# Optimization experiments

Measured on AMD Instinct MI355X. Metric: run time of the kernel, lower is better.

The kernel has to match this reference:

```python
import jax, jax.numpy as jnp
import numpy as np

N_HEAD, D_K, D_V, D_MODEL = 8, 64, 64, 512
LN_EPS = 1e-5

def setup_inputs() -> dict:
    key = jax.random.key(0)
    k1, k2, k3 = jax.random.split(key, 3)
    B, C, H, W = 8, D_MODEL, 32, 32
    q = jax.random.normal(k1, (B, C, H, W), dtype=jnp.float32)
    w_qkvs = jax.random.normal(k2, (N_HEAD * D_K, D_MODEL), dtype=jnp.float32) * np.sqrt(2.0 / (D_MODEL + D_K))
    fc_w = jax.random.normal(k3, (D_MODEL, N_HEAD * D_V), dtype=jnp.float32) * np.sqrt(2.0 / (N_HEAD * D_V + D_MODEL))
    fc_b = jnp.zeros((D_MODEL,), dtype=jnp.float32)
    ln_gamma = jnp.ones((D_MODEL,), dtype=jnp.float32)
    ln_beta = jnp.zeros((D_MODEL,), dtype=jnp.float32)
    return {"q": q, "w_qkvs": w_qkvs, "fc_w": fc_w, "fc_b": fc_b,
            "ln_gamma": ln_gamma, "ln_beta": ln_beta}

def reference(q, w_qkvs, fc_w, fc_b, ln_gamma, ln_beta):
    B, C, H, W = q.shape
    L = H * W
    temp = np.sqrt(D_K).astype(np.float32)
    # [B, C, H, W] -> [B, L, C] tokens
    x = q.reshape(B, C, L).transpose(0, 2, 1)
    residual = x
    # shared QKV projection -> per-head [B, h, L, d]
    qh = (x @ w_qkvs.T).reshape(B, L, N_HEAD, D_K).transpose(0, 2, 1, 3)
    # self-attention: q = k = v = qh
    scores = jnp.einsum('bhqd,bhkd->bhqk', qh, qh) / temp
    attn = jax.nn.softmax(scores, axis=-1)  # dropout is identity in eval
    out = jnp.einsum('bhqk,bhkd->bhqd', attn, qh)  # [B, h, L, d_v]
    # merge heads: [B, L, h*d_v]
    out = out.transpose(0, 2, 1, 3).reshape(B, L, N_HEAD * D_V)
    out = out @ fc_w.T + fc_b
    y = out + residual
    mu = jnp.mean(y, axis=-1, keepdims=True)
    var = jnp.mean(jnp.square(y - mu), axis=-1, keepdims=True)
    y = (y - mu) / jnp.sqrt(var + LN_EPS) * ln_gamma + ln_beta
    # raw reshape, matching torch .view(B, -1, H, W)
    return y.reshape(B, -1, H, W)
```

## Files before the change

kernel.cpp:

```cpp
#include <hip/hip_runtime.h>
#include <stdint.h>

#define BATCH 8
#define LTOK 1024
#define DMODEL 512
#define NHEAD 8
#define DHEAD 64

typedef unsigned short u16;
typedef u16 u16x4 __attribute__((ext_vector_type(4)));
typedef u16 u16x8 __attribute__((ext_vector_type(8)));
typedef short bf16x8 __attribute__((ext_vector_type(8)));
typedef float f32x4 __attribute__((ext_vector_type(4)));

#define MFMA16(a,b,c) __builtin_amdgcn_mfma_f32_16x16x32_bf16((a),(b),(c),0,0,0)

__device__ __forceinline__ float bf2f(u16 x){
  union{unsigned u; float f;} v; v.u = ((unsigned)x)<<16; return v.f;
}
__device__ __forceinline__ u16 f2bf(float f){
  union{float f; unsigned u;} v; v.f = f;
  unsigned r = v.u + 0x7fffu + ((v.u>>16)&1u);
  return (u16)(r>>16);
}

__device__ __forceinline__ void gload_lds16(const u16* g, u16* l){
  __builtin_amdgcn_global_load_lds(
      (const __attribute__((address_space(1))) void*)g,
      (__attribute__((address_space(3))) void*)l,
      16, 0, 0);
}

__global__ __launch_bounds__(256) void prep_k(const float* __restrict__ q,
                                              u16* __restrict__ x_rm,
                                              const float* __restrict__ w0,
                                              u16* __restrict__ d0,
                                              const float* __restrict__ w1,
                                              u16* __restrict__ d1){
  __shared__ __align__(16) u16 t[64][72];
  const int blk = blockIdx.x;
  const int tid = threadIdx.x;
  if (blk < 1024){
    const int bx = blk & 7, by = (blk>>3) & 15, bz = blk>>7;
    const int r0 = bx*64, c0 = by*64;
    const float* s = q    + (size_t)bz*DMODEL*LTOK;
    u16* d         = x_rm + (size_t)bz*DMODEL*LTOK;
    const int row = tid>>3, ch = (tid&7)*8;
    #pragma unroll
    for (int rr=0; rr<64; rr+=32){
      const float* p = s + (size_t)(r0+row+rr)*LTOK + c0 + ch;
      u16x8 v;
      #pragma unroll
      for (int j=0;j<8;j++) v[j] = f2bf(p[j]);
      *(u16x8*)&t[row+rr][ch] = v;
    }
    __syncthreads();
    #pragma unroll
    for (int rr=0; rr<64; rr+=32){
      const int dr = row+rr;
      u16x8 v;
      #pragma unroll
      for (int j=0;j<8;j++) v[j] = t[ch+j][dr];
      *(u16x8*)(d + (size_t)(c0+dr)*DMODEL + r0 + ch) = v;
    }
  } else {
    const int b2 = blk - 1024;
    const float* src = (b2 < 128) ? w0 : w1;
    u16* dst        = (b2 < 128) ? d0 : d1;
    const int i = (((b2 & 127)*256) + tid)*8;
    u16x8 v;
    #pragma unroll
    for (int j=0;j<8;j++) v[j] = f2bf(src[i+j]);
    *(u16x8*)(dst + i) = v;
  }
}

__device__ __forceinline__ void stage128(const u16* __restrict__ src,
                                         int row0, int k0, u16* lds, int tid){
  #pragma unroll
  for (int s2=0; s2<4; ++s2){
    const int slot = tid + s2*256;
    const int row = slot>>3, ch8 = slot&7;
    const int k = k0 + ((ch8 ^ (row&7))<<3);
    gload_lds16(src + (size_t)(row0+row)*DMODEL + k, lds + slot*8);
  }
}

__global__ __launch_bounds__(256) void qkv_gemm(const u16* __restrict__ A,
                                                const u16* __restrict__ W,
                                                u16* __restrict__ Kf,
                                                u16* __restrict__ Vf){
  __shared__ __align__(128) u16 smem[32768];
  const int m0 = blockIdx.x*128, n0 = blockIdx.y*128;
  const int tid = threadIdx.x, w = tid>>6, lane = tid&63;
  const int wr = w>>1, wc = w&1;
  const int lr = lane&15, lg = lane>>4;
  f32x4 acc[4][4] = {};
  stage128(A, m0, 0, smem, tid);
  stage128(W, n0, 0, smem + 16384, tid);
  int buf = 0;
  for (int kt=0; kt<8; ++kt){
    __syncthreads();
    if (kt < 7){
      stage128(A, m0, (kt+1)*64, smem + (buf^1)*8192, tid);
      stage128(W, n0, (kt+1)*64, smem + 16384 + (buf^1)*8192, tid);
    }
    const u16* sa = smem + buf*8192;
    const u16* sb = smem + 16384 + buf*8192;
    #pragma unroll
    for (int ks=0; ks<2; ++ks){
      bf16x8 af[4], bfr[4];
      #pragma unroll
      for (int mi=0; mi<4; ++mi){
        const int r = wr*64 + mi*16 + lr;
        af[mi] = *(const bf16x8*)(&sa[(r*64 + ks*32 + lg*8) ^ ((r&7)<<3)]);
      }
      #pragma unroll
      for (int nj=0; nj<4; ++nj){
        const int r = wc*64 + nj*16 + lr;
        bfr[nj] = *(const bf16x8*)(&sb[(r*64 + ks*32 + lg*8) ^ ((r&7)<<3)]);
      }
      #pragma unroll
      for (int mi=0; mi<4; ++mi)
        #pragma unroll
        for (int nj=0; nj<4; ++nj)
          acc[mi][nj] = MFMA16(af[mi], bfr[nj], acc[mi][nj]);
    }
    buf ^= 1;
  }
  __syncthreads();
  u16* Ktile = smem + w*4096;
  u16* Vtile = smem + 16384 + w*4096;
  #pragma unroll
  for (int mi=0; mi<4; ++mi)
    #pragma unroll
    for (int nj=0; nj<4; ++nj){
      const int rrb = mi*16 + lg*4;
      const int d   = nj*16 + lr;
      #pragma unroll
      for (int r=0; r<4; ++r){
        const int rr = rrb + r;
        Ktile[((d>>5)*4 + (rr>>4))*512 + (((d>>3)&3)*16 + (rr&15))*8 + (d&7)]
            = f2bf(acc[mi][nj][r]);
      }
      u16x4 pv;
      #pragma unroll
      for (int r=0; r<4; ++r) pv[r] = f2bf(acc[mi][nj][r]);
      *(u16x4*)&Vtile[((rrb>>5)*4 + (d>>4))*512 + (((rrb>>3)&3)*16 + (d&15))*8 + (rrb&7)] = pv;
    }
  __syncthreads();
  const int bb = m0>>10, t0 = (m0&1023)>>6, hh0 = n0>>6;
  #pragma unroll
  for (int p=0; p<8; ++p){
    const int gi = p*2048 + tid*8;
    const int lt = gi>>12, off = gi&4095;
    const size_t base = (size_t)((bb*NHEAD + hh0 + (lt&1))*16 + t0 + (lt>>1))*4096 + off;
    *(u16x8*)(Kf + base) = *(const u16x8*)(smem + gi);
    *(u16x8*)(Vf + base) = *(const u16x8*)(smem + 16384 + gi);
  }
}

__global__ __launch_bounds__(256,2) void attn_k(const u16* __restrict__ kf,
                                                const u16* __restrict__ vf,
                                                u16* __restrict__ ao){
  __shared__ __align__(16) u16 sPm[16640];
  const int bid = blockIdx.x;
  const int qt = bid >> 6, bh = bid & 63;
  const int b = bh >> 3, h = bh & 7;
  const u16* Kf = kf + (size_t)bh*16*4096;
  const u16* Vf = vf + (size_t)bh*16*4096;
  const int tid = threadIdx.x, w = tid>>6, lane = tid&63;
  const int lr = lane&15, lg = lane>>4;

  bf16x8 aq[4][2];
  #pragma unroll
  for (int g=0; g<4; ++g)
    #pragma unroll
    for (int ks=0; ks<2; ++ks){
      u16x8 v = *(const u16x8*)(Kf + (size_t)qt*4096 + (ks*4+g)*512 + lane*8);
      bf16x8 t;
      #pragma unroll
      for (int j=0;j<8;j++) t[j] = (short)f2bf(bf2f(v[j])*0.18033688f);
      aq[g][ks] = t;
    }

  f32x4 o[4][4] = {};
  float lsum[4][4] = {};

  for (int t=0; t<4; ++t){
    const int kt = w + t*4;
    const u16* Kt = Kf + (size_t)kt*4096;
    const u16* Vt = Vf + (size_t)kt*4096;
    bf16x8 bk[2][4];
    #pragma unroll
    for (int ks=0; ks<2; ++ks)
      #pragma unroll
      for (int nj=0; nj<4; ++nj)
        bk[ks][nj] = *(const bf16x8*)(Kt + (ks*4+nj)*512 + lane*8);
    #pragma unroll
    for (int g=0; g<4; ++g){
      f32x4 sc[4] = {};
      __builtin_amdgcn_s_setprio(1);
      #pragma unroll
      for (int ks=0; ks<2; ++ks)
        #pragma unroll
        for (int nj=0; nj<4; ++nj)
          sc[nj] = MFMA16(aq[g][ks], bk[ks][nj], sc[nj]);
      __builtin_amdgcn_s_setprio(0);
      const int wp = (w*4+g)*1024;
      #pragma unroll
      for (int nj=0; nj<4; ++nj){
        #pragma unroll
        for (int r=0; r<4; ++r){
          const float p = __builtin_amdgcn_exp2f(sc[nj][r]);
          lsum[g][r] += p;
          const int prow = lg*4 + r;
          sPm[wp + ((prow*64 + nj*16 + lr) ^ ((prow&7)<<3))]
              = (u16)(__float_as_uint(p)>>16);
        }
      }
    }
    asm volatile("s_waitcnt lgkmcnt(0)" ::: "memory");
    bf16x8 bv[2][4];
    #pragma unroll
    for (int ks=0; ks<2; ++ks)
      #pragma unroll
      for (int dj=0; dj<4; ++dj)
        bv[ks][dj] = *(const bf16x8*)(Vt + (ks*4+dj)*512 + lane*8);
    __builtin_amdgcn_s_setprio(1);
    #pragma unroll
    for (int g=0; g<4; ++g){
      const int wp = (w*4+g)*1024;
      #pragma unroll
      for (int ks=0; ks<2; ++ks){
        bf16x8 pa = *(const bf16x8*)(&sPm[wp + ((lr*64 + ks*32 + lg*8) ^ ((lr&7)<<3))]);
        #pragma unroll
        for (int dj=0; dj<4; ++dj)
          o[g][dj] = MFMA16(pa, bv[ks][dj], o[g][dj]);
      }
    }
    __builtin_amdgcn_s_setprio(0);
  }

  #pragma unroll
  for (int g=0; g<4; ++g)
    #pragma unroll
    for (int r=0; r<4; ++r){
      float s = lsum[g][r];
      s += __shfl_xor(s,1); s += __shfl_xor(s,2);
      s += __shfl_xor(s,4); s += __shfl_xor(s,8);
      lsum[g][r] = s;
    }

  __syncthreads();
  float* mrg = (float*)sPm;
  if (w & 1){
    float* R = mrg + (w>>1)*4160;
    #pragma unroll
    for (int g=0; g<4; ++g){
      #pragma unroll
      for (int dj=0; dj<4; ++dj)
        *(f32x4*)&R[(g*4+dj)*256 + lane*4] = o[g][dj];
      if (lr == 0)
        #pragma unroll
        for (int r=0; r<4; ++r) R[4096 + g*16 + lg*4 + r] = lsum[g][r];
    }
  }
  __syncthreads();
  if (!(w & 1)){
    float* R = mrg + (w>>1)*4160;
    #pragma unroll
    for (int g=0; g<4; ++g){
      #pragma unroll
      for (int dj=0; dj<4; ++dj)
        o[g][dj] += *(const f32x4*)&R[(g*4+dj)*256 + lane*4];
      #pragma unroll
      for (int r=0; r<4; ++r) lsum[g][r] += R[4096 + g*16 + lg*4 + r];
    }
  }
  if (w == 2){
    float* R = mrg + 4160;
    #pragma unroll
    for (int g=0; g<4; ++g){
      #pragma unroll
      for (int dj=0; dj<4; ++dj)
        *(f32x4*)&R[(g*4+dj)*256 + lane*4] = o[g][dj];
      if (lr == 0)
        #pragma unroll
        for (int r=0; r<4; ++r) R[4096 + g*16 + lg*4 + r] = lsum[g][r];
    }
  }
  __syncthreads();
  if (w == 0){
    float* R = mrg + 4160;
    #pragma unroll
    for (int g=0; g<4; ++g){
      #pragma unroll
      for (int dj=0; dj<4; ++dj)
        o[g][dj] += *(const f32x4*)&R[(g*4+dj)*256 + lane*4];
      #pragma unroll
      for (int r=0; r<4; ++r) lsum[g][r] += R[4096 + g*16 + lg*4 + r];
    }
    #pragma unroll
    for (int g=0; g<4; ++g){
      float inv[4];
      #pragma unroll
      for (int r=0; r<4; ++r) inv[r] = __builtin_amdgcn_rcpf(lsum[g][r]);
      const int i0 = qt*64 + g*16;
      #pragma unroll
      for (int dj=0; dj<4; ++dj)
        #pragma unroll
        for (int r=0; r<4; ++r){
          const int l = i0 + lg*4 + r;
          const int d = dj*16 + lr;
          ao[((size_t)(b*LTOK + l))*DMODEL + h*DHEAD + d] = f2bf(o[g][dj][r]*inv[r]);
        }
    }
  }
}

__global__ __launch_bounds__(256) void fc_gemm(const u16* __restrict__ A,
                                               const u16* __restrict__ W,
                                               const float* __restrict__ bias,
                                               const u16* __restrict__ resid,
                                               u16* __restrict__ Y){
  __shared__ __align__(128) u16 smem[32768];
  const int m0 = blockIdx.x*128, n0 = blockIdx.y*128;
  const int tid = threadIdx.x, w = tid>>6, lane = tid&63;
  const int wr = w>>1, wc = w&1;
  const int lr = lane&15, lg = lane>>4;
  f32x4 acc[4][4] = {};
  stage128(A, m0, 0, smem, tid);
  stage128(W, n0, 0, smem + 16384, tid);
  int buf = 0;
  for (int kt=0; kt<8; ++kt){
    __syncthreads();
    if (kt < 7){
      stage128(A, m0, (kt+1)*64, smem + (buf^1)*8192, tid);
      stage128(W, n0, (kt+1)*64, smem + 16384 + (buf^1)*8192, tid);
    }
    const u16* sa = smem + buf*8192;
    const u16* sb = smem + 16384 + buf*8192;
    #pragma unroll
    for (int ks=0; ks<2; ++ks){
      bf16x8 af[4], bfr[4];
      #pragma unroll
      for (int mi=0; mi<4; ++mi){
        const int r = wr*64 + mi*16 + lr;
        af[mi] = *(const bf16x8*)(&sa[(r*64 + ks*32 + lg*8) ^ ((r&7)<<3)]);
      }
      #pragma unroll
      for (int nj=0; nj<4; ++nj){
        const int r = wc*64 + nj*16 + lr;
        bfr[nj] = *(const bf16x8*)(&sb[(r*64 + ks*32 + lg*8) ^ ((r&7)<<3)]);
      }
      #pragma unroll
      for (int mi=0; mi<4; ++mi)
        #pragma unroll
        for (int nj=0; nj<4; ++nj)
          acc[mi][nj] = MFMA16(af[mi], bfr[nj], acc[mi][nj]);
    }
    buf ^= 1;
  }
  __syncthreads();
  float* lY = (float*)smem;
  #pragma unroll
  for (int mi=0; mi<4; ++mi)
    #pragma unroll
    for (int nj=0; nj<4; ++nj)
      #pragma unroll
      for (int r=0; r<4; ++r){
        const int rr = wr*64 + mi*16 + lg*4 + r;
        const int d  = wc*64 + nj*16 + lr;
        lY[rr*128 + (d ^ ((rr&7)<<2))] = acc[mi][nj][r];
      }
  __syncthreads();
  #pragma unroll
  for (int p=0; p<8; ++p){
    const int slot = p*256 + tid;
    const int row = slot>>4;
    const int ch  = (slot&15)*8;
    const int x   = (row&7)<<2;
    f32x4 ya = *(const f32x4*)&lY[row*128 + (ch ^ x)];
    f32x4 yb = *(const f32x4*)&lY[row*128 + ((ch+4) ^ x)];
    u16x8 rs = *(const u16x8*)(resid + (size_t)(m0+row)*DMODEL + n0 + ch);
    u16x8 o8;
    #pragma unroll
    for (int j=0;j<4;j++) o8[j]   = f2bf(ya[j] + bias[n0+ch+j]   + bf2f(rs[j]));
    #pragma unroll
    for (int j=0;j<4;j++) o8[j+4] = f2bf(yb[j] + bias[n0+ch+4+j] + bf2f(rs[j+4]));
    *(u16x8*)(Y + (size_t)(m0+row)*DMODEL + n0 + ch) = o8;
  }
}

__global__ __launch_bounds__(256) void ln_k(const u16* __restrict__ Y,
                                            const float* __restrict__ gamma,
                                            const float* __restrict__ beta,
                                            float* __restrict__ out){
  const int row = blockIdx.x*4 + (threadIdx.x>>6);
  const int lane = threadIdx.x&63;
  const u16* yr = Y + (size_t)row*DMODEL;
  u16x8 v = *(const u16x8*)(yr + lane*8);
  float x[8]; float s=0.f, sq=0.f;
  #pragma unroll
  for (int j=0;j<8;j++){ x[j]=bf2f(v[j]); s+=x[j]; sq+=x[j]*x[j]; }
  #pragma unroll
  for (int mk=1; mk<64; mk<<=1){ s += __shfl_xor(s,mk); sq += __shfl_xor(sq,mk); }
  const float mean = s*(1.f/DMODEL);
  float var = sq*(1.f/DMODEL) - mean*mean;
  const float rstd = rsqrtf(var + 1e-5f);
  float* po = out + (size_t)row*DMODEL + lane*8;
  #pragma unroll
  for (int j=0;j<8;j++){
    const int c = lane*8+j;
    po[j] = (x[j]-mean)*rstd*gamma[c] + beta[c];
  }
}

extern "C" void kernel_launch(void* const* d_in, const int* in_sizes, int n_in,
                              void* d_out, int out_size, void* d_ws, size_t ws_size,
                              hipStream_t stream){
  (void)in_sizes; (void)n_in; (void)out_size; (void)ws_size;
  const float* q      = (const float*)d_in[0];
  const float* w_qkvs = (const float*)d_in[1];
  const float* fc_w   = (const float*)d_in[2];
  const float* fc_b   = (const float*)d_in[3];
  const float* ln_g   = (const float*)d_in[4];
  const float* ln_b   = (const float*)d_in[5];
  float* out = (float*)d_out;
  char* ws = (char*)d_ws;
  u16* x_rm  = (u16*)(ws);
  u16* kfb   = (u16*)(ws + 8388608);
  u16* vfb   = (u16*)(ws + 16777216);
  u16* ao    = (u16*)(ws + 25165824);
  u16* wqkvb = (u16*)(ws + 33554432);
  u16* wfcb  = (u16*)(ws + 34078720);
  u16* y0    = kfb;

  prep_k<<<1280,256,0,stream>>>(q, x_rm, w_qkvs, wqkvb, fc_w, wfcb);
  qkv_gemm<<<dim3(64,4),256,0,stream>>>(x_rm, wqkvb, kfb, vfb);
  attn_k<<<1024,256,0,stream>>>(kfb, vfb, ao);
  fc_gemm<<<dim3(64,4),256,0,stream>>>(ao, wfcb, fc_b, x_rm, y0);
  ln_k<<<2048,256,0,stream>>>(y0, ln_g, ln_b, out);
}
```

Before: 68.89 us.

## Fuse FC projection with residual and LayerNorm using pre-laid-out weight fragments

Merges the output-projection GEMM and the LayerNorm into one kernel. Each block computes 32 full rows of 512 columns, so the residual add and normalization run from LDS without writing an intermediate bf16 Y to global memory and launching a separate kernel. The prep kernel now stores fc weights in an MFMA-fragment-ordered layout so each wave loads B operands straight from global/L2 without LDS staging. The trade-off is only 256 blocks, fewer rows per block, and B fragments re-read from global memory by every block.

Result: slower. 71.60 us (+3.9%).

```diff
diff --git a/kernel.cpp b/kernel.cpp
--- a/kernel.cpp
+++ b/kernel.cpp
@@ -63,15 +63,24 @@
       for (int j=0;j<8;j++) v[j] = t[ch+j][dr];
       *(u16x8*)(d + (size_t)(c0+dr)*DMODEL + r0 + ch) = v;
     }
+  } else if (blk < 1152){
+    const int b2 = blk - 1024;
+    const int i = ((b2*256) + tid)*8;
+    u16x8 v;
+    #pragma unroll
+    for (int j=0;j<8;j++) v[j] = f2bf(w0[i+j]);
+    *(u16x8*)(d0 + i) = v;
   } else {
-    const int b2 = blk - 1024;
-    const float* src = (b2 < 128) ? w0 : w1;
-    u16* dst        = (b2 < 128) ? d0 : d1;
-    const int i = (((b2 & 127)*256) + tid)*8;
+    const int b2 = blk - 1152;
+    const int i = ((b2*256) + tid)*8;
+    const int n = i>>9, k = i&511;
     u16x8 v;
     #pragma unroll
-    for (int j=0;j<8;j++) v[j] = f2bf(src[i+j]);
-    *(u16x8*)(dst + i) = v;
+    for (int j=0;j<8;j++) v[j] = f2bf(w1[i+j]);
+    const int nt = n>>6, kt = k>>6;
+    const int dst = (nt*8 + kt)*4096 + (((k>>5)&1)*4 + ((n>>4)&3))*512
+                  + (((k>>3)&3)*16 + (n&15))*8;
+    *(u16x8*)(d1 + dst) = v;
   }
 }
 
@@ -319,101 +328,101 @@
   }
 }
 
-__global__ __launch_bounds__(256) void fc_gemm(const u16* __restrict__ A,
-                                               const u16* __restrict__ W,
+__global__ __launch_bounds__(256,2) void fc_ln(const u16* __restrict__ A,
+                                               const u16* __restrict__ Wf,
                                                const float* __restrict__ bias,
                                                const u16* __restrict__ resid,
-                                               u16* __restrict__ Y){
-  __shared__ __align__(128) u16 smem[32768];
-  const int m0 = blockIdx.x*128, n0 = blockIdx.y*128;
+                                               const float* __restrict__ gamma,
+                                               const float* __restrict__ beta,
+                                               float* __restrict__ out){
+  __shared__ __align__(128) u16 sA[2][2048];
+  __shared__ __align__(16)  u16 sY[32*520];
+  const int m0 = blockIdx.x*32;
   const int tid = threadIdx.x, w = tid>>6, lane = tid&63;
-  const int wr = w>>1, wc = w&1;
   const int lr = lane&15, lg = lane>>4;
-  f32x4 acc[4][4] = {};
-  stage128(A, m0, 0, smem, tid);
-  stage128(W, n0, 0, smem + 16384, tid);
+
+  f32x4 acc[2][8] = {};
+  {
+    const int row = tid>>3, ch8 = tid&7;
+    gload_lds16(A + (size_t)(m0+row)*DMODEL + ((ch8 ^ (row&7))<<3), sA[0] + tid*8);
+  }
   int buf = 0;
   for (int kt=0; kt<8; ++kt){
     __syncthreads();
     if (kt < 7){
-      stage128(A, m0, (kt+1)*64, smem + (buf^1)*8192, tid);
-      stage128(W, n0, (kt+1)*64, smem + 16384 + (buf^1)*8192, tid);
-    }
-    const u16* sa = smem + buf*8192;
-    const u16* sb = smem + 16384 + buf*8192;
+      const int row = tid>>3, ch8 = tid&7;
+      gload_lds16(A + (size_t)(m0+row)*DMODEL + (kt+1)*64 + ((ch8 ^ (row&7))<<3),
+                  sA[buf^1] + tid*8);
+    }
+    bf16x8 bfr[2][8];
+    #pragma unroll
+    for (int ks=0; ks<2; ++ks)
+      #pragma unroll
+      for (int nj=0; nj<8; ++nj){
+        const int nt = w*2 + (nj>>2);
+        bfr[ks][nj] = *(const bf16x8*)(Wf + (size_t)(nt*8 + kt)*4096
+                                       + (ks*4 + (nj&3))*512 + lane*8);
+      }
     #pragma unroll
     for (int ks=0; ks<2; ++ks){
-      bf16x8 af[4], bfr[4];
-      #pragma unroll
-      for (int mi=0; mi<4; ++mi){
-        const int r = wr*64 + mi*16 + lr;
-        af[mi] = *(const bf16x8*)(&sa[(r*64 + ks*32 + lg*8) ^ ((r&7)<<3)]);
-      }
-      #pragma unroll
-      for (int nj=0; nj<4; ++nj){
-        const int r = wc*64 + nj*16 + lr;
-        bfr[nj] = *(const bf16x8*)(&sb[(r*64 + ks*32 + lg*8) ^ ((r&7)<<3)]);
-      }
-      #pragma unroll
-      for (int mi=0; mi<4; ++mi)
-        #pragma unroll
-        for (int nj=0; nj<4; ++nj)
-          acc[mi][nj] = MFMA16(af[mi], bfr[nj], acc[mi][nj]);
+      bf16x8 af[2];
+      #pragma unroll
+      for (int mi=0; mi<2; ++mi){
+        const int r = mi*16 + lr;
+        af[mi] = *(const bf16x8*)(&sA[buf][(r*64 + ks*32 + lg*8) ^ ((r&7)<<3)]);
+      }
+      #pragma unroll
+      for (int mi=0; mi<2; ++mi)
+        #pragma unroll
+        for (int nj=0; nj<8; ++nj)
+          acc[mi][nj] = MFMA16(af[mi], bfr[ks][nj], acc[mi][nj]);
     }
     buf ^= 1;
   }
   __syncthreads();
-  float* lY = (float*)smem;
-  #pragma unroll
-  for (int mi=0; mi<4; ++mi)
-    #pragma unroll
-    for (int nj=0; nj<4; ++nj)
+  #pragma unroll
+  for (int mi=0; mi<2; ++mi)
+    #pragma unroll
+    for (int nj=0; nj<8; ++nj){
+      const int d = w*128 + nj*16 + lr;
       #pragma unroll
       for (int r=0; r<4; ++r){
-        const int rr = wr*64 + mi*16 + lg*4 + r;
-        const int d  = wc*64 + nj*16 + lr;
-        lY[rr*128 + (d ^ ((rr&7)<<2))] = acc[mi][nj][r];
-      }
-  __syncthreads();
-  #pragma unroll
-  for (int p=0; p<8; ++p){
-    const int slot = p*256 + tid;
-    const int row = slot>>4;
-    const int ch  = (slot&15)*8;
-    const int x   = (row&7)<<2;
-    f32x4 ya = *(const f32x4*)&lY[row*128 + (ch ^ x)];
-    f32x4 yb = *(const f32x4*)&lY[row*128 + ((ch+4) ^ x)];
-    u16x8 rs = *(const u16x8*)(resid + (size_t)(m0+row)*DMODEL + n0 + ch);
-    u16x8 o8;
-    #pragma unroll
-    for (int j=0;j<4;j++) o8[j]   = f2bf(ya[j] + bias[n0+ch+j]   + bf2f(rs[j]));
-    #pragma unroll
-    for (int j=0;j<4;j++) o8[j+4] = f2bf(yb[j] + bias[n0+ch+4+j] + bf2f(rs[j+4]));
-    *(u16x8*)(Y + (size_t)(m0+row)*DMODEL + n0 + ch) = o8;
-  }
-}
-
-__global__ __launch_bounds__(256) void ln_k(const u16* __restrict__ Y,
-                                            const float* __restrict__ gamma,
-                                            const float* __restrict__ beta,
-                                            float* __restrict__ out){
-  const int row = blockIdx.x*4 + (threadIdx.x>>6);
-  const int lane = threadIdx.x&63;
-  const u16* yr = Y + (size_t)row*DMODEL;
-  u16x8 v = *(const u16x8*)(yr + lane*8);
-  float x[8]; float s=0.f, sq=0.f;
-  #pragma unroll
-  for (int j=0;j<8;j++){ x[j]=bf2f(v[j]); s+=x[j]; sq+=x[j]*x[j]; }
-  #pragma unroll
-  for (int mk=1; mk<64; mk<<=1){ s += __shfl_xor(s,mk); sq += __shfl_xor(sq,mk); }
-  const float mean = s*(1.f/DMODEL);
-  float var = sq*(1.f/DMODEL) - mean*mean;
-  const float rstd = rsqrtf(var + 1e-5f);
-  float* po = out + (size_t)row*DMODEL + lane*8;
-  #pragma unroll
-  for (int j=0;j<8;j++){
-    const int c = lane*8+j;
-    po[j] = (x[j]-mean)*rstd*gamma[c] + beta[c];
+        const int rr = mi*16 + lg*4 + r;
+        sY[rr*520 + d] = f2bf(acc[mi][nj][r]);
+      }
+    }
+  __syncthreads();
+  const float g0a = gamma[lane*8+0], g1 = gamma[lane*8+1], g2 = gamma[lane*8+2],
+              g3 = gamma[lane*8+3], g4 = gamma[lane*8+4], g5 = gamma[lane*8+5],
+              g6 = gamma[lane*8+6], g7 = gamma[lane*8+7];
+  const float b0 = beta[lane*8+0], b1 = beta[lane*8+1], b2 = beta[lane*8+2],
+              b3 = beta[lane*8+3], b4 = beta[lane*8+4], b5 = beta[lane*8+5],
+              b6 = beta[lane*8+6], b7 = beta[lane*8+7];
+  const float bi0 = bias[lane*8+0], bi1 = bias[lane*8+1], bi2 = bias[lane*8+2],
+              bi3 = bias[lane*8+3], bi4 = bias[lane*8+4], bi5 = bias[lane*8+5],
+              bi6 = bias[lane*8+6], bi7 = bias[lane*8+7];
+  const float gm[8] = {g0a,g1,g2,g3,g4,g5,g6,g7};
+  const float bt[8] = {b0,b1,b2,b3,b4,b5,b6,b7};
+  const float bi[8] = {bi0,bi1,bi2,bi3,bi4,bi5,bi6,bi7};
+  #pragma unroll
+  for (int i=0; i<8; ++i){
+    const int rr = w*8 + i;
+    u16x8 yv = *(const u16x8*)&sY[rr*520 + lane*8];
+    u16x8 rv = *(const u16x8*)(resid + (size_t)(m0+rr)*DMODEL + lane*8);
+    float x[8]; float s=0.f, sq=0.f;
+    #pragma unroll
+    for (int j=0;j<8;j++){
+      x[j] = bf2f(yv[j]) + bi[j] + bf2f(rv[j]);
+      s += x[j]; sq += x[j]*x[j];
+    }
+    #pragma unroll
+    for (int mk=1; mk<64; mk<<=1){ s += __shfl_xor(s,mk); sq += __shfl_xor(sq,mk); }
+    const float mean = s*(1.f/DMODEL);
+    const float var = sq*(1.f/DMODEL) - mean*mean;
+    const float rstd = rsqrtf(var + 1e-5f);
+    float* po = out + (size_t)(m0+rr)*DMODEL + lane*8;
+    #pragma unroll
+    for (int j=0;j<8;j++) po[j] = (x[j]-mean)*rstd*gm[j] + bt[j];
   }
 }
 
@@ -434,12 +443,10 @@
   u16* vfb   = (u16*)(ws + 16777216);
   u16* ao    = (u16*)(ws + 25165824);
   u16* wqkvb = (u16*)(ws + 33554432);
-  u16* wfcb  = (u16*)(ws + 34078720);
-  u16* y0    = kfb;
-
-  prep_k<<<1280,256,0,stream>>>(q, x_rm, w_qkvs, wqkvb, fc_w, wfcb);
+  u16* wfcf  = (u16*)(ws + 34078720);
+
+  prep_k<<<1280,256,0,stream>>>(q, x_rm, w_qkvs, wqkvb, fc_w, wfcf);
   qkv_gemm<<<dim3(64,4),256,0,stream>>>(x_rm, wqkvb, kfb, vfb);
   attn_k<<<1024,256,0,stream>>>(kfb, vfb, ao);
-  fc_gemm<<<dim3(64,4),256,0,stream>>>(ao, wfcb, fc_b, x_rm, y0);
-  ln_k<<<2048,256,0,stream>>>(y0, ln_g, ln_b, out);
-}
+  fc_ln<<<256,256,0,stream>>>(ao, wfcf, fc_b, x_rm, ln_g, ln_b, out);
+}
```
